# Kernel tuning notes

Measured on AMD Instinct MI355X. Metric: run time of the kernel, lower is better.

## Reference

```python
import jax, jax.numpy as jnp
import numpy as np

B, N, DIN, DOUT = 8, 2048, 128, 128

def setup_inputs() -> dict:
    key = jax.random.key(0)
    k1, k2, k3, k4 = jax.random.split(key, 4)
    x = jax.random.normal(k1, (B, N, DIN), dtype=jnp.float32)
    adj = jax.random.uniform(k2, (B, N, N), dtype=jnp.float32)
    W = jax.random.normal(k3, (DIN, DOUT), dtype=jnp.float32) / np.sqrt(DIN)
    b = jax.random.normal(k4, (DOUT,), dtype=jnp.float32) * 0.01
    return {"x": x, "adj": adj, "W": W, "b": b}

def reference(x, adj, W, b):
    # degree over last dim of adj: [B, N]
    degree = jnp.sum(adj, axis=2)
    d_norm = 1.0 / jnp.sqrt(degree + 1e-8)
    # D^{-1/2} A D^{-1/2} == row/col elementwise scaling (same math as diag_embed+bmm)
    adj_norm = d_norm[:, :, None] * adj * d_norm[:, None, :]
    support = jnp.einsum('bnm,bmd->bnd', adj_norm, x)  # [B, N, DIN]
    return support @ W + b  # [B, N, DOUT]
```

## Files before the change

kernel.cpp:

```cpp
#include <hip/hip_runtime.h>
#include <hip/hip_bf16.h>

#define NN 2048
#define DD 128

typedef __attribute__((ext_vector_type(4))) float f32x4;
typedef __attribute__((ext_vector_type(8))) short short8;

__device__ __forceinline__ unsigned short f2bf_bits(float f) {
  union { __hip_bfloat16 h; unsigned short s; } u;
  u.h = __float2bfloat16(f);
  return u.s;
}

__device__ __forceinline__ short8 cvt8(f32x4 a, f32x4 b) {
  short8 r;
  r[0] = (short)f2bf_bits(a[0]); r[1] = (short)f2bf_bits(a[1]);
  r[2] = (short)f2bf_bits(a[2]); r[3] = (short)f2bf_bits(a[3]);
  r[4] = (short)f2bf_bits(b[0]); r[5] = (short)f2bf_bits(b[1]);
  r[6] = (short)f2bf_bits(b[2]); r[7] = (short)f2bf_bits(b[3]);
  return r;
}

__device__ __forceinline__ void gld16(const void* src, void* lds) {
  __builtin_amdgcn_global_load_lds(
      (const __attribute__((address_space(1))) void*)src,
      (__attribute__((address_space(3))) void*)lds, 16, 0, 0);
}

__global__ void k_degree(const float* __restrict__ adj, float* __restrict__ dnorm) {
  const int wv = threadIdx.x >> 6;
  const int ln = threadIdx.x & 63;
  const int row = blockIdx.x * 4 + wv;
  const f32x4* rowp = (const f32x4*)(adj + (size_t)row * NN);
  float s = 0.0f;
#pragma unroll
  for (int i = 0; i < 8; ++i) {
    f32x4 v = rowp[i * 64 + ln];
    s += v[0] + v[1] + v[2] + v[3];
  }
#pragma unroll
  for (int off = 32; off >= 1; off >>= 1) s += __shfl_xor(s, off);
  if (ln == 0) dnorm[row] = rsqrtf(s + 1e-8f);
}

__global__ void k_y(const float* __restrict__ x, const float* __restrict__ W,
                    const float* __restrict__ dnorm, short* __restrict__ yT) {
  const int ln = threadIdx.x & 63;
  const int wv = threadIdx.x >> 6;
  const int bb = blockIdx.x >> 5;
  const int n0 = (blockIdx.x & 31) << 6;
  const int l15 = ln & 15, l4 = ln >> 4;
  const int dbase = wv * 32;

  short8 af[2][4];
#pragma unroll
  for (int dt = 0; dt < 2; ++dt)
#pragma unroll
    for (int ks = 0; ks < 4; ++ks) {
      short8 a;
#pragma unroll
      for (int j = 0; j < 8; ++j)
        a[j] = (short)f2bf_bits(W[(size_t)(ks * 32 + l4 * 8 + j) * DD + dbase + dt * 16 + l15]);
      af[dt][ks] = a;
    }

  f32x4 acc[2][4];
#pragma unroll
  for (int dt = 0; dt < 2; ++dt)
#pragma unroll
    for (int nt = 0; nt < 4; ++nt) acc[dt][nt] = (f32x4)0.0f;

  const float* xb = x + (size_t)bb * NN * DD;
  const float* dnb = dnorm + (size_t)bb * NN;
#pragma unroll
  for (int nt = 0; nt < 4; ++nt) {
    const int n = n0 + nt * 16 + l15;
    const float dn = dnb[n];
#pragma unroll
    for (int ks = 0; ks < 4; ++ks) {
      f32x4 p = *(const f32x4*)(xb + (size_t)n * DD + ks * 32 + l4 * 8);
      f32x4 q = *(const f32x4*)(xb + (size_t)n * DD + ks * 32 + l4 * 8 + 4);
      short8 bf = cvt8(p * dn, q * dn);
#pragma unroll
      for (int dt = 0; dt < 2; ++dt)
        acc[dt][nt] = __builtin_amdgcn_mfma_f32_16x16x32_bf16(af[dt][ks], bf, acc[dt][nt], 0, 0, 0);
    }
  }

  short* yb = yT + (size_t)bb * DD * NN;
#pragma unroll
  for (int dt = 0; dt < 2; ++dt)
#pragma unroll
    for (int nt = 0; nt < 4; ++nt)
#pragma unroll
      for (int rr = 0; rr < 4; ++rr) {
        int d = dbase + dt * 16 + l4 * 4 + rr;
        yb[(size_t)d * NN + n0 + nt * 16 + l15] = (short)f2bf_bits(acc[dt][nt][rr]);
      }
}

__launch_bounds__(512, 1)
__global__ void k_gemm4(const float* __restrict__ adj, const short* __restrict__ yT,
                        const float* __restrict__ dnorm, const float* __restrict__ bias,
                        float* __restrict__ out) {
  __shared__ char As[2][65536];

  const int t = threadIdx.x;
  const int ln = t & 63;
  const int wv = t >> 6;
  const int l15 = ln & 15, l4 = ln >> 4;
  const int orig = ((blockIdx.x & 7) << 5) | (blockIdx.x >> 3);
  const int bb = orig >> 5;
  const int m0 = (orig & 31) << 6;

  const char* ablk = (const char*)(adj + ((size_t)bb * NN + m0) * NN);
  const int oc = (wv << 4) + l15;
  const int kg8 = l4 << 3;
  const short* ybase = yT + ((size_t)bb * DD + oc) * NN;

  f32x4 acc[4];
#pragma unroll
  for (int m = 0; m < 4; ++m) acc[m] = (f32x4)0.0f;

  auto stage = [&](int S, int buf) {
#pragma unroll
    for (int i = 0; i < 8; ++i) {
      const int row = (wv << 3) + i;
      const char* src = ablk + (size_t)row * (NN * 4) + (size_t)S * 1024 +
                        (((unsigned)(ln ^ (i & 7))) << 4);
      gld16(src, (char*)As + (buf << 16) + ((unsigned)row << 10));
    }
  };
  auto loadB = [&](int S, short8 B[8]) {
#pragma unroll
    for (int kk = 0; kk < 8; ++kk)
      B[kk] = *(const short8*)(ybase + S * 256 + kk * 32 + kg8);
  };
  auto compute = [&](int buf, short8 B[8]) {
    const char* base = (const char*)As + (buf << 16);
#pragma unroll
    for (int kk = 0; kk < 8; ++kk) {
#pragma unroll
      for (int m = 0; m < 4; ++m) {
        const unsigned row = (unsigned)(m * 16 + l15);
        const unsigned s = row & 7u;
        const unsigned q0 = (unsigned)(kk * 8 + l4 * 2);
        f32x4 f0 = *(const f32x4*)(base + (row << 10) + ((q0 ^ s) << 4));
        f32x4 f1 = *(const f32x4*)(base + (row << 10) + (((q0 + 1) ^ s) << 4));
        acc[m] = __builtin_amdgcn_mfma_f32_16x16x32_bf16(cvt8(f0, f1), B[kk], acc[m], 0, 0, 0);
      }
    }
  };

  short8 E[8], O[8];
  stage(0, 0);
  loadB(0, E);
  asm volatile("s_waitcnt vmcnt(0)\n\ts_barrier" ::: "memory");

#pragma unroll 1
  for (int S2 = 0; S2 < 8; S2 += 2) {
    if (S2 + 1 < 8) { stage(S2 + 1, (S2 + 1) & 1); loadB(S2 + 1, O); }
    compute(S2 & 1, E);
    if (S2 + 1 < 8)
      asm volatile("s_waitcnt vmcnt(8)\n\ts_barrier" ::: "memory");
    if (S2 + 1 < 8) {
      if (S2 + 2 < 8) { stage(S2 + 2, (S2 + 2) & 1); loadB(S2 + 2, E); }
      compute((S2 + 1) & 1, O);
      if (S2 + 2 < 8)
        asm volatile("s_waitcnt vmcnt(8)\n\ts_barrier" ::: "memory");
    }
  }

  const float bv = bias[oc];
  const int rbase = l4 << 2;
#pragma unroll
  for (int m = 0; m < 4; ++m) {
    f32x4 dn = *(const f32x4*)(dnorm + (size_t)bb * NN + m0 + m * 16 + rbase);
#pragma unroll
    for (int rr = 0; rr < 4; ++rr)
      out[(size_t)(bb * NN + m0 + m * 16 + rbase + rr) * DD + oc] = acc[m][rr] * dn[rr] + bv;
  }
}

extern "C" void kernel_launch(void* const* d_in, const int* in_sizes, int n_in,
                              void* d_out, int out_size, void* d_ws, size_t ws_size,
                              hipStream_t stream) {
  (void)in_sizes; (void)n_in; (void)out_size; (void)ws_size;
  const float* x = (const float*)d_in[0];
  const float* adj = (const float*)d_in[1];
  const float* W = (const float*)d_in[2];
  const float* bias = (const float*)d_in[3];
  float* out = (float*)d_out;

  char* ws = (char*)d_ws;
  float* dnorm = (float*)ws;
  short* yT = (short*)(ws + (1 << 16));

  k_degree<<<4096, 256, 0, stream>>>(adj, dnorm);
  k_y<<<256, 256, 0, stream>>>(x, W, dnorm, yT);
  k_gemm4<<<256, 512, 0, stream>>>(adj, yT, dnorm, bias, out);
}
```

Measured before the change: 67.32 us.

## Halve GEMM row tile to 32 rows, double grid, two blocks per CU

The main adj×y GEMM now uses 32-row tiles instead of 64, launching 512 blocks with 32 KB LDS buffers and allowing two blocks per CU. Waves are remapped so each handles one 16-row slice and two 16-column output groups, reusing each converted A fragment for two MFMAs. The aim is better occupancy and latency hiding on the memory-bound adj stream. In exchange, each y tile is loaded by twice as many blocks, and register pressure rises from holding four B fragment arrays.

```diff
diff --git a/kernel.cpp b/kernel.cpp
--- a/kernel.cpp
+++ b/kernel.cpp
@@ -100,86 +100,90 @@
       }
 }
 
-__launch_bounds__(512, 1)
-__global__ void k_gemm4(const float* __restrict__ adj, const short* __restrict__ yT,
+__launch_bounds__(512, 2)
+__global__ void k_gemm5(const float* __restrict__ adj, const short* __restrict__ yT,
                         const float* __restrict__ dnorm, const float* __restrict__ bias,
                         float* __restrict__ out) {
-  __shared__ char As[2][65536];
+  __shared__ char As[2][32768];
 
   const int t = threadIdx.x;
   const int ln = t & 63;
   const int wv = t >> 6;
   const int l15 = ln & 15, l4 = ln >> 4;
-  const int orig = ((blockIdx.x & 7) << 5) | (blockIdx.x >> 3);
-  const int bb = orig >> 5;
-  const int m0 = (orig & 31) << 6;
+  const int ms = wv >> 2;
+  const int dq = wv & 3;
+  const int orig = ((blockIdx.x & 7) << 6) | (blockIdx.x >> 3);
+  const int bb = orig >> 6;
+  const int m0 = (orig & 63) << 5;
 
   const char* ablk = (const char*)(adj + ((size_t)bb * NN + m0) * NN);
-  const int oc = (wv << 4) + l15;
+  const int oc0 = (dq << 5) + l15;
+  const int oc1 = oc0 + 16;
   const int kg8 = l4 << 3;
-  const short* ybase = yT + ((size_t)bb * DD + oc) * NN;
-
-  f32x4 acc[4];
-#pragma unroll
-  for (int m = 0; m < 4; ++m) acc[m] = (f32x4)0.0f;
+  const short* yb0 = yT + ((size_t)bb * DD + oc0) * NN + kg8;
+  const short* yb1 = yT + ((size_t)bb * DD + oc1) * NN + kg8;
+
+  f32x4 acc0 = (f32x4)0.f, acc1 = (f32x4)0.f;
 
   auto stage = [&](int S, int buf) {
 #pragma unroll
-    for (int i = 0; i < 8; ++i) {
-      const int row = (wv << 3) + i;
+    for (int i = 0; i < 4; ++i) {
+      const int row = (wv << 2) + i;
       const char* src = ablk + (size_t)row * (NN * 4) + (size_t)S * 1024 +
-                        (((unsigned)(ln ^ (i & 7))) << 4);
-      gld16(src, (char*)As + (buf << 16) + ((unsigned)row << 10));
+                        (((unsigned)(ln ^ (row & 7))) << 4);
+      gld16(src, (char*)As + (buf << 15) + ((unsigned)row << 10));
     }
   };
-  auto loadB = [&](int S, short8 B[8]) {
-#pragma unroll
-    for (int kk = 0; kk < 8; ++kk)
-      B[kk] = *(const short8*)(ybase + S * 256 + kk * 32 + kg8);
+  auto loadB = [&](int S, short8 B0[8], short8 B1[8]) {
+#pragma unroll
+    for (int kk = 0; kk < 8; ++kk) {
+      B0[kk] = *(const short8*)(yb0 + S * 256 + kk * 32);
+      B1[kk] = *(const short8*)(yb1 + S * 256 + kk * 32);
+    }
   };
-  auto compute = [&](int buf, short8 B[8]) {
-    const char* base = (const char*)As + (buf << 16);
+  auto compute = [&](int buf, short8 B0[8], short8 B1[8]) {
+    const char* base = (const char*)As + (buf << 15);
+    const unsigned row = (unsigned)((ms << 4) + l15);
+    const unsigned s = row & 7u;
+    const char* rbase = base + (row << 10);
 #pragma unroll
     for (int kk = 0; kk < 8; ++kk) {
-#pragma unroll
-      for (int m = 0; m < 4; ++m) {
-        const unsigned row = (unsigned)(m * 16 + l15);
-        const unsigned s = row & 7u;
-        const unsigned q0 = (unsigned)(kk * 8 + l4 * 2);
-        f32x4 f0 = *(const f32x4*)(base + (row << 10) + ((q0 ^ s) << 4));
-        f32x4 f1 = *(const f32x4*)(base + (row << 10) + (((q0 + 1) ^ s) << 4));
-        acc[m] = __builtin_amdgcn_mfma_f32_16x16x32_bf16(cvt8(f0, f1), B[kk], acc[m], 0, 0, 0);
-      }
+      const unsigned q0 = (unsigned)(kk * 8 + l4 * 2);
+      f32x4 f0 = *(const f32x4*)(rbase + ((q0 ^ s) << 4));
+      f32x4 f1 = *(const f32x4*)(rbase + (((q0 + 1) ^ s) << 4));
+      short8 af = cvt8(f0, f1);
+      acc0 = __builtin_amdgcn_mfma_f32_16x16x32_bf16(af, B0[kk], acc0, 0, 0, 0);
+      acc1 = __builtin_amdgcn_mfma_f32_16x16x32_bf16(af, B1[kk], acc1, 0, 0, 0);
     }
   };
 
-  short8 E[8], O[8];
+  short8 E0[8], E1[8], O0[8], O1[8];
   stage(0, 0);
-  loadB(0, E);
+  loadB(0, E0, E1);
   asm volatile("s_waitcnt vmcnt(0)\n\ts_barrier" ::: "memory");
 
 #pragma unroll 1
   for (int S2 = 0; S2 < 8; S2 += 2) {
-    if (S2 + 1 < 8) { stage(S2 + 1, (S2 + 1) & 1); loadB(S2 + 1, O); }
-    compute(S2 & 1, E);
-    if (S2 + 1 < 8)
-      asm volatile("s_waitcnt vmcnt(8)\n\ts_barrier" ::: "memory");
+    if (S2 + 1 < 8) { stage(S2 + 1, 1); loadB(S2 + 1, O0, O1); }
+    compute(0, E0, E1);
     if (S2 + 1 < 8) {
-      if (S2 + 2 < 8) { stage(S2 + 2, (S2 + 2) & 1); loadB(S2 + 2, E); }
-      compute((S2 + 1) & 1, O);
+      asm volatile("s_waitcnt vmcnt(16)\n\ts_barrier" ::: "memory");
+      if (S2 + 2 < 8) { stage(S2 + 2, 0); loadB(S2 + 2, E0, E1); }
+      compute(1, O0, O1);
       if (S2 + 2 < 8)
-        asm volatile("s_waitcnt vmcnt(8)\n\ts_barrier" ::: "memory");
-    }
-  }
-
-  const float bv = bias[oc];
-  const int rbase = l4 << 2;
-#pragma unroll
-  for (int m = 0; m < 4; ++m) {
-    f32x4 dn = *(const f32x4*)(dnorm + (size_t)bb * NN + m0 + m * 16 + rbase);
-#pragma unroll
-    for (int rr = 0; rr < 4; ++rr)
-      out[(size_t)(bb * NN + m0 + m * 16 + rbase + rr) * DD + oc] = acc[m][rr] * dn[rr] + bv;
+        asm volatile("s_waitcnt vmcnt(16)\n\ts_barrier" ::: "memory");
+    }
+  }
+
+  const float bv0 = bias[oc0];
+  const float bv1 = bias[oc1];
+  const int rb = (ms << 4) + (l4 << 2);
+  f32x4 dn4 = *(const f32x4*)(dnorm + (size_t)bb * NN + m0 + rb);
+#pragma unroll
+  for (int rr = 0; rr < 4; ++rr) {
+    const size_t base = (size_t)(bb * NN + m0 + rb + rr) * DD;
+    out[base + oc0] = acc0[rr] * dn4[rr] + bv0;
+    out[base + oc1] = acc1[rr] * dn4[rr] + bv1;
   }
 }
 
@@ -199,5 +203,5 @@
 
   k_degree<<<4096, 256, 0, stream>>>(adj, dnorm);
   k_y<<<256, 256, 0, stream>>>(x, W, dnorm, yT);
-  k_gemm4<<<256, 512, 0, stream>>>(adj, yT, dnorm, bias, out);
-}
+  k_gemm5<<<512, 512, 0, stream>>>(adj, yT, dnorm, bias, out);
+}
```

Result: slower. 107.5 us (+59.6%).
